# Optimization experiments

Measured on AMD Instinct MI355X. Metric: run time of the kernel, lower is better.

## Reference

```python
import jax, jax.numpy as jnp
import numpy as np
import math

D, S, B = 64, 2048, 16  # head_dim, seq_len, batch (inputs stored as [D, S, B])


def setup_inputs() -> dict:
    key = jax.random.key(0)
    kq, kk, kv = jax.random.split(key, 3)
    return {
        "Q": jax.random.normal(kq, (D, S, B), dtype=jnp.float32),
        "K": jax.random.normal(kk, (D, S, B), dtype=jnp.float32),
        "V": jax.random.normal(kv, (D, S, B), dtype=jnp.float32),
        "d_k": S,
    }


def reference(Q, K, V, d_k):
    # transpose(0, 2): [D, S, B] -> [B, S, D]
    q = jnp.transpose(Q, (2, 1, 0))
    k = jnp.transpose(K, (2, 1, 0))
    v = jnp.transpose(V, (2, 1, 0))
    # bmm(_Q, K_T) * 1/sqrt(d_k): [B, S, S]
    scores = jnp.einsum("bsd,btd->bst", q, k) * (1.0 / math.sqrt(d_k))
    # original does view(-1, d_k) + Softmax over dim=1; with d_k == last dim
    # this is a softmax over the key axis. Dropout is identity in eval mode.
    probs = jax.nn.softmax(scores, axis=-1)
    out = jnp.einsum("bst,btd->bsd", probs, v)  # [B, S, D]
    # transpose(0, 2) back: [D, S, B]
    return jnp.transpose(out, (2, 1, 0))
```

## Files before the change

kernel.cpp:

```cpp
#include <hip/hip_runtime.h>

#define D_ 64
#define S_ 2048
#define B_ 16
#define QT 64
#define KVT 128

typedef short short8 __attribute__((ext_vector_type(8)));
typedef short short4a __attribute__((ext_vector_type(4)));
typedef float floatx4 __attribute__((ext_vector_type(4)));
typedef unsigned uint2v __attribute__((ext_vector_type(2)));

#define SC2 (1.4426950408889634f / 45.254833995939045f)

__device__ __forceinline__ unsigned short f2bf(float f) {
  unsigned u = __builtin_bit_cast(unsigned, f);
  u += 0x7fffu + ((u >> 16) & 1u);
  return (unsigned short)(u >> 16);
}

__device__ __forceinline__ floatx4 mfma16(short4a a, short4a b, floatx4 c) {
#if __has_builtin(__builtin_amdgcn_mfma_f32_16x16x16bf16_1k)
  return __builtin_amdgcn_mfma_f32_16x16x16bf16_1k(a, b, c, 0, 0, 0);
#else
  floatx4 d;
  asm volatile("v_mfma_f32_16x16x16_bf16 %0, %1, %2, %3"
               : "=v"(d) : "v"(a), "v"(b), "v"(c));
  return d;
#endif
}

__global__ __launch_bounds__(256) void pack_all(const float* __restrict__ Q,
                                                const float* __restrict__ K,
                                                const float* __restrict__ V,
                                                unsigned short* __restrict__ Qp,
                                                unsigned short* __restrict__ Kp,
                                                unsigned short* __restrict__ Vt) {
  __shared__ __align__(16) unsigned short tile[256][72];
  const int t = threadIdx.x;
  const int bid = blockIdx.x;
  if (bid < 256) {
    const bool isK = bid >= 128;
    const float* src = isK ? K : Q;
    unsigned short* dst = isK ? Kp : Qp;
    const float scale = isK ? SC2 : 1.0f;
    const int s0 = (bid & 127) * 16;
#pragma unroll
    for (int i = 0; i < 16; i++) {
      int j = i * 256 + t;
      int d = j >> 6;
      int sb4 = (j & 63) * 4;
      const float4 v = *(const float4*)(src + (size_t)d * (S_ * B_) + s0 * B_ + sb4);
      float vv[4] = {v.x, v.y, v.z, v.w};
#pragma unroll
      for (int k = 0; k < 4; k++) {
        int sb = sb4 + k;
        tile[(sb & 15) * 16 + (sb >> 4)][d] = f2bf(vv[k] * scale);
      }
    }
    __syncthreads();
#pragma unroll
    for (int i = 0; i < 8; i++) {
      int j = i * 256 + t;
      int r = j >> 3, c = j & 7;
      int b = r >> 4, si = r & 15;
      uint4 v = *(const uint4*)(&tile[r][c * 8]);
      *(uint4*)(dst + ((size_t)(b * S_ + s0 + si) * D_ + c * 8)) = v;
    }
  } else {
    const int vb = bid - 256;
    const int s0 = (vb & 31) * 64;
    const int d0 = (vb >> 5) * 16;
#pragma unroll
    for (int i = 0; i < 16; i++) {
      int j = i * 256 + t;
      int dd = j >> 8;
      int sb4 = (j & 255) * 4;
      const float4 v = *(const float4*)(V + (size_t)(d0 + dd) * (S_ * B_) + s0 * B_ + sb4);
      float vv[4] = {v.x, v.y, v.z, v.w};
#pragma unroll
      for (int k = 0; k < 4; k++) {
        int sb = sb4 + k;
        tile[(sb & 15) * 16 + dd][sb >> 4] = f2bf(vv[k]);
      }
    }
    __syncthreads();
#pragma unroll
    for (int i = 0; i < 8; i++) {
      int j = i * 256 + t;
      int r = j >> 3, c = j & 7;
      int b = r >> 4, dd = r & 15;
      uint4 v = *(const uint4*)(&tile[r][c * 8]);
      *(uint4*)(Vt + ((size_t)(b * D_ + d0 + dd) * S_ + s0 + c * 8)) = v;
    }
  }
}

__global__ __launch_bounds__(256, 2) void attn(const unsigned short* __restrict__ Qp,
                                               const unsigned short* __restrict__ Kp,
                                               const unsigned short* __restrict__ Vt,
                                               float* __restrict__ Ot) {
  __shared__ __align__(16) char smem_[69632 + 1024];
  float* red = (float*)smem_;
  float* lred = (float*)(smem_ + 69632);
  unsigned short* Vbuf0 = (unsigned short*)smem_;
  unsigned short* Vbuf1 = (unsigned short*)(smem_ + 17408);

  const int tid = threadIdx.x;
  const int w = tid >> 6, l = tid & 63, g = l >> 4, ln = l & 15;
  const int b = blockIdx.x & 15;
  const int q0 = (int)(blockIdx.x >> 4) * QT;
  const int kvw = w * 32;

  const unsigned short* Qb = Qp + (size_t)b * S_ * D_;
  const unsigned short* Kb = Kp + (size_t)b * S_ * D_;
  const unsigned short* Vb = Vt + (size_t)b * D_ * S_;

  short8 qf[4][2];
#pragma unroll
  for (int nf = 0; nf < 4; nf++)
#pragma unroll
    for (int ks = 0; ks < 2; ks++)
      qf[nf][ks] = *(const short8*)(Qb + (size_t)(q0 + nf * 16 + ln) * D_ + ks * 32 + g * 8);

  short8 kf[2][2];
#pragma unroll
  for (int mf = 0; mf < 2; mf++)
#pragma unroll
    for (int ks = 0; ks < 2; ks++)
      kf[mf][ks] = *(const short8*)(Kb + (size_t)(kvw + mf * 16 + ln) * D_ + ks * 32 + g * 8);

  {
    uint4 vstg[4];
#pragma unroll
    for (int i = 0; i < 4; i++) {
      int idx = i * 256 + tid, r = idx >> 4, c = idx & 15;
      vstg[i] = *(const uint4*)(Vb + (size_t)r * S_ + c * 8);
    }
#pragma unroll
    for (int i = 0; i < 4; i++) {
      int idx = i * 256 + tid, r = idx >> 4, c = idx & 15;
      *(uint4*)(&Vbuf0[r * 136 + c * 8]) = vstg[i];
    }
  }
  __syncthreads();

  const short4a ones = {(short)0x3F80, (short)0x3F80, (short)0x3F80, (short)0x3F80};
  floatx4 oacc[4][4];
  floatx4 dacc[4];
#pragma unroll
  for (int mfd = 0; mfd < 4; mfd++)
#pragma unroll
    for (int nf = 0; nf < 4; nf++) oacc[mfd][nf] = (floatx4){0.f, 0.f, 0.f, 0.f};
#pragma unroll
  for (int nf = 0; nf < 4; nf++) dacc[nf] = (floatx4){0.f, 0.f, 0.f, 0.f};

  for (int t = 0; t < 16; t++) {
    const int kvn = ((t + 1) * KVT) & (S_ - 1);

    uint4 vstg[4];
#pragma unroll
    for (int i = 0; i < 4; i++) {
      int idx = i * 256 + tid, r = idx >> 4, c = idx & 15;
      vstg[i] = *(const uint4*)(Vb + (size_t)r * S_ + kvn + c * 8);
    }

    floatx4 sacc[2][4];
#pragma unroll
    for (int mf = 0; mf < 2; mf++)
#pragma unroll
      for (int nf = 0; nf < 4; nf++) sacc[mf][nf] = (floatx4){0.f, 0.f, 0.f, 0.f};
#pragma unroll
    for (int ks = 0; ks < 2; ks++)
#pragma unroll
      for (int mf = 0; mf < 2; mf++)
#pragma unroll
        for (int nf = 0; nf < 4; nf++)
          sacc[mf][nf] = __builtin_amdgcn_mfma_f32_16x16x32_bf16(kf[mf][ks], qf[nf][ks],
                                                                 sacc[mf][nf], 0, 0, 0);

#pragma unroll
    for (int mf = 0; mf < 2; mf++)
#pragma unroll
      for (int ks = 0; ks < 2; ks++)
        kf[mf][ks] = *(const short8*)(Kb + (size_t)(kvn + kvw + mf * 16 + ln) * D_ + ks * 32 + g * 8);

    short4a pb[2][4];
#pragma unroll
    for (int mf = 0; mf < 2; mf++)
#pragma unroll
      for (int nf = 0; nf < 4; nf++) {
        unsigned u0 = __builtin_bit_cast(unsigned, __builtin_amdgcn_exp2f(sacc[mf][nf][0])) + 0x8000u;
        unsigned u1 = __builtin_bit_cast(unsigned, __builtin_amdgcn_exp2f(sacc[mf][nf][1])) + 0x8000u;
        unsigned u2 = __builtin_bit_cast(unsigned, __builtin_amdgcn_exp2f(sacc[mf][nf][2])) + 0x8000u;
        unsigned u3 = __builtin_bit_cast(unsigned, __builtin_amdgcn_exp2f(sacc[mf][nf][3])) + 0x8000u;
        unsigned lo = __builtin_amdgcn_perm(u1, u0, 0x07060302u);
        unsigned hi = __builtin_amdgcn_perm(u3, u2, 0x07060302u);
        pb[mf][nf] = __builtin_bit_cast(short4a, (uint2v){lo, hi});
      }

#pragma unroll
    for (int mf = 0; mf < 2; mf++)
#pragma unroll
      for (int nf = 0; nf < 4; nf++)
        dacc[nf] = mfma16(ones, pb[mf][nf], dacc[nf]);

    unsigned short* vw = ((t + 1) & 1) ? Vbuf1 : Vbuf0;
#pragma unroll
    for (int i = 0; i < 4; i++) {
      int idx = i * 256 + tid, r = idx >> 4, c = idx & 15;
      *(uint4*)(&vw[r * 136 + c * 8]) = vstg[i];
    }

    const unsigned short* vr = (t & 1) ? Vbuf1 : Vbuf0;
#pragma unroll
    for (int mfd = 0; mfd < 4; mfd++)
#pragma unroll
      for (int mf = 0; mf < 2; mf++) {
        short4a vf = *(const short4a*)(&vr[(mfd * 16 + ln) * 136 + kvw + mf * 16 + g * 4]);
#pragma unroll
        for (int nf = 0; nf < 4; nf++)
          oacc[mfd][nf] = mfma16(vf, pb[mf][nf], oacc[mfd][nf]);
      }
    __syncthreads();
  }

  if (g == 0) {
#pragma unroll
    for (int nf = 0; nf < 4; nf++) lred[w * 64 + nf * 16 + ln] = dacc[nf][0];
  }
#pragma unroll
  for (int mfd = 0; mfd < 4; mfd++)
#pragma unroll
    for (int nf = 0; nf < 4; nf++)
      *(floatx4*)(&red[w * 4352 + (nf * 16 + ln) * 68 + mfd * 16 + g * 4]) = oacc[mfd][nf];
  __syncthreads();

  const int q = l;
  const float denom = lred[q] + lred[64 + q] + lred[128 + q] + lred[192 + q];
  const float linv = 1.0f / denom;
#pragma unroll
  for (int i = 0; i < 4; i++) {
    floatx4 s = (floatx4){0.f, 0.f, 0.f, 0.f};
#pragma unroll
    for (int w2 = 0; w2 < 4; w2++)
      s += *(const floatx4*)(&red[w2 * 4352 + q * 68 + w * 16 + i * 4]);
    s *= linv;
#pragma unroll
    for (int r = 0; r < 4; r++)
      Ot[(size_t)(b * D_ + w * 16 + i * 4 + r) * S_ + q0 + q] = s[r];
  }
}

__global__ __launch_bounds__(256) void unpack_o(const float* __restrict__ Ot,
                                                float* __restrict__ out) {
  const int d0 = (int)(blockIdx.x & 7) * 8;
  const int s0 = (int)(blockIdx.x >> 3) * 64;
  __shared__ float u[8 * 1024];
  const int t = threadIdx.x;
#pragma unroll
  for (int i = 0; i < 8; i++) {
    int j = i * 256 + t;
    int d = j >> 8, bb = (j >> 4) & 15, c = j & 15;
    float4 v = *(const float4*)(Ot + (size_t)(bb * D_ + d0 + d) * S_ + s0 + c * 4);
    float vv[4] = {v.x, v.y, v.z, v.w};
#pragma unroll
    for (int k = 0; k < 4; k++) {
      int si = c * 4 + k;
      int W = si * 16 + bb;
      int Wp = W ^ ((si & 15) << 2);
      u[d * 1024 + Wp] = vv[k];
    }
  }
  __syncthreads();
#pragma unroll
  for (int i = 0; i < 8; i++) {
    int j = i * 256 + t;
    int d = j >> 8, c2 = j & 255;
    int G = c2 ^ ((c2 >> 2) & 15);
    float4 v = *(const float4*)(&u[d * 1024 + G * 4]);
    *(float4*)(out + (size_t)(d0 + d) * (S_ * B_) + s0 * B_ + c2 * 4) = v;
  }
}

extern "C" void kernel_launch(void* const* d_in, const int* in_sizes, int n_in,
                              void* d_out, int out_size, void* d_ws, size_t ws_size,
                              hipStream_t stream) {
  const float* Q = (const float*)d_in[0];
  const float* K = (const float*)d_in[1];
  const float* V = (const float*)d_in[2];
  float* out = (float*)d_out;
  char* ws = (char*)d_ws;
  unsigned short* Qp = (unsigned short*)(ws);
  unsigned short* Kp = (unsigned short*)(ws + (4u << 20));
  unsigned short* Vt = (unsigned short*)(ws + (8u << 20));
  float* Ot = (float*)(ws + (12u << 20));

  hipLaunchKernelGGL(pack_all, dim3(384), dim3(256), 0, stream, Q, K, V, Qp, Kp, Vt);
  hipLaunchKernelGGL(attn, dim3(512), dim3(256), 0, stream, Qp, Kp, Vt, Ot);
  hipLaunchKernelGGL(unpack_o, dim3(256), dim3(256), 0, stream, Ot, out);
}
```

Baseline: 111.3 us.

## Load V fragments directly from global into registers, drop LDS double buffer

Each wave now loads its own V MFMA fragments straight from global memory into registers, prefetching the next tile after the PV MFMAs. This removes the shared-memory V staging, the LDS writes and reads, and the per-iteration __syncthreads. It also wraps the MFMA sections in s_setprio to favour matrix issue across waves. In exchange, the per-lane global loads are narrow 8-byte strided reads with less coalescing, and register pressure rises.

```diff
diff --git a/kernel.cpp b/kernel.cpp
--- a/kernel.cpp
+++ b/kernel.cpp
@@ -103,8 +103,6 @@
   __shared__ __align__(16) char smem_[69632 + 1024];
   float* red = (float*)smem_;
   float* lred = (float*)(smem_ + 69632);
-  unsigned short* Vbuf0 = (unsigned short*)smem_;
-  unsigned short* Vbuf1 = (unsigned short*)(smem_ + 17408);
 
   const int tid = threadIdx.x;
   const int w = tid >> 6, l = tid & 63, g = l >> 4, ln = l & 15;
@@ -130,20 +128,13 @@
     for (int ks = 0; ks < 2; ks++)
       kf[mf][ks] = *(const short8*)(Kb + (size_t)(kvw + mf * 16 + ln) * D_ + ks * 32 + g * 8);
 
-  {
-    uint4 vstg[4];
-#pragma unroll
-    for (int i = 0; i < 4; i++) {
-      int idx = i * 256 + tid, r = idx >> 4, c = idx & 15;
-      vstg[i] = *(const uint4*)(Vb + (size_t)r * S_ + c * 8);
-    }
-#pragma unroll
-    for (int i = 0; i < 4; i++) {
-      int idx = i * 256 + tid, r = idx >> 4, c = idx & 15;
-      *(uint4*)(&Vbuf0[r * 136 + c * 8]) = vstg[i];
-    }
-  }
-  __syncthreads();
+  const unsigned short* Vw = Vb + (size_t)ln * S_ + kvw + g * 4;
+  short4a vf[4][2];
+#pragma unroll
+  for (int mfd = 0; mfd < 4; mfd++)
+#pragma unroll
+    for (int mf = 0; mf < 2; mf++)
+      vf[mfd][mf] = *(const short4a*)(Vw + (size_t)(mfd * 16) * S_ + mf * 16);
 
   const short4a ones = {(short)0x3F80, (short)0x3F80, (short)0x3F80, (short)0x3F80};
   floatx4 oacc[4][4];
@@ -158,18 +149,12 @@
   for (int t = 0; t < 16; t++) {
     const int kvn = ((t + 1) * KVT) & (S_ - 1);
 
-    uint4 vstg[4];
-#pragma unroll
-    for (int i = 0; i < 4; i++) {
-      int idx = i * 256 + tid, r = idx >> 4, c = idx & 15;
-      vstg[i] = *(const uint4*)(Vb + (size_t)r * S_ + kvn + c * 8);
-    }
-
     floatx4 sacc[2][4];
 #pragma unroll
     for (int mf = 0; mf < 2; mf++)
 #pragma unroll
       for (int nf = 0; nf < 4; nf++) sacc[mf][nf] = (floatx4){0.f, 0.f, 0.f, 0.f};
+    __builtin_amdgcn_s_setprio(1);
 #pragma unroll
     for (int ks = 0; ks < 2; ks++)
 #pragma unroll
@@ -178,6 +163,7 @@
         for (int nf = 0; nf < 4; nf++)
           sacc[mf][nf] = __builtin_amdgcn_mfma_f32_16x16x32_bf16(kf[mf][ks], qf[nf][ks],
                                                                  sacc[mf][nf], 0, 0, 0);
+    __builtin_amdgcn_s_setprio(0);
 
 #pragma unroll
     for (int mf = 0; mf < 2; mf++)
@@ -199,30 +185,28 @@
         pb[mf][nf] = __builtin_bit_cast(short4a, (uint2v){lo, hi});
       }
 
+    __builtin_amdgcn_s_setprio(1);
 #pragma unroll
     for (int mf = 0; mf < 2; mf++)
 #pragma unroll
       for (int nf = 0; nf < 4; nf++)
         dacc[nf] = mfma16(ones, pb[mf][nf], dacc[nf]);
 
-    unsigned short* vw = ((t + 1) & 1) ? Vbuf1 : Vbuf0;
-#pragma unroll
-    for (int i = 0; i < 4; i++) {
-      int idx = i * 256 + tid, r = idx >> 4, c = idx & 15;
-      *(uint4*)(&vw[r * 136 + c * 8]) = vstg[i];
-    }
-
-    const unsigned short* vr = (t & 1) ? Vbuf1 : Vbuf0;
 #pragma unroll
     for (int mfd = 0; mfd < 4; mfd++)
 #pragma unroll
       for (int mf = 0; mf < 2; mf++) {
-        short4a vf = *(const short4a*)(&vr[(mfd * 16 + ln) * 136 + kvw + mf * 16 + g * 4]);
 #pragma unroll
         for (int nf = 0; nf < 4; nf++)
-          oacc[mfd][nf] = mfma16(vf, pb[mf][nf], oacc[mfd][nf]);
-      }
-    __syncthreads();
+          oacc[mfd][nf] = mfma16(vf[mfd][mf], pb[mf][nf], oacc[mfd][nf]);
+      }
+    __builtin_amdgcn_s_setprio(0);
+
+#pragma unroll
+    for (int mfd = 0; mfd < 4; mfd++)
+#pragma unroll
+      for (int mf = 0; mf < 2; mf++)
+        vf[mfd][mf] = *(const short4a*)(Vw + (size_t)(mfd * 16) * S_ + kvn + mf * 16);
   }
 
   if (g == 0) {
```

Result: slower. 130.7 us (+17.4%).
